# Performance work log

Hardware: AMD Instinct MI355X
Metric: run time of the kernel (lower is better)

## Reference

```python
import jax, jax.numpy as jnp
import numpy as np


def setup_inputs() -> dict:
    key = jax.random.key(0)
    B, D, C, H = 4096, 64, 128, 512
    ks = jax.random.split(key, 6)
    return {
        "q_z_x_params": jax.random.normal(ks[0], (B, C), jnp.float32),
        "eps": jax.random.normal(ks[1], (B, D), jnp.float32),
        "W1": jax.random.normal(ks[2], (D + C, H), jnp.float32) / np.sqrt(D + C).astype(np.float32),
        "b1": jnp.zeros((H,), jnp.float32),
        "W2": jax.random.normal(ks[3], (H, H), jnp.float32) / np.sqrt(H).astype(np.float32),
        "b2": jnp.zeros((H,), jnp.float32),
        "W3": jax.random.normal(ks[4], (H, 2 * D), jnp.float32) / np.sqrt(H).astype(np.float32),
        "b3": jnp.zeros((2 * D,), jnp.float32),
    }


def _made_masks(D, C, H):
    # Standard MADE degrees, natural ordering; context columns fully connected.
    m_in = np.arange(1, D + 1)                      # input degrees 1..D
    m_h = (np.arange(H) % (D - 1)) + 1              # hidden degrees 1..D-1
    M1 = np.concatenate([m_h[None, :] >= m_in[:, None],
                         np.ones((C, H), bool)], axis=0)   # (D+C, H)
    M2 = m_h[None, :] >= m_h[:, None]               # (H, H)
    m_out = np.tile(np.arange(1, D + 1), 2)         # (2D,) mean||prescale
    M3 = m_out[None, :] > m_h[:, None]              # (H, 2D)
    f32 = jnp.float32
    return jnp.asarray(M1, f32), jnp.asarray(M2, f32), jnp.asarray(M3, f32)


def reference(q_z_x_params, eps, W1, b1, W2, b2, W3, b3):
    B, D = eps.shape
    C = q_z_x_params.shape[1]
    H = W2.shape[0]
    M1, M2, M3 = _made_masks(D, C, H)
    mW1, mW2, mW3 = W1 * M1, W2 * M2, W3 * M3

    def made(z):
        x = jnp.concatenate([z, q_z_x_params], axis=1)   # (B, D+C)
        h1 = jax.nn.relu(x @ mW1 + b1)
        h2 = jax.nn.relu(h1 @ mW2 + b2)
        out = h2 @ mW3 + b3                              # (B, 2D)
        return out[:, :D], out[:, D:]

    def step(z, i):
        mean, prescale = made(z)
        mu_i = jnp.take(mean, i, axis=1)                 # (B,)
        scale_i = jax.nn.softplus(jnp.take(prescale, i, axis=1))
        z_i = mu_i + scale_i * jnp.take(eps, i, axis=1)  # reparameterized Normal sample
        z = z.at[:, i].set(z_i)
        return z, None

    z0 = jnp.zeros((B, D), eps.dtype)
    z_sample, _ = jax.lax.scan(step, z0, jnp.arange(D))
    return z_sample
```

## Files before the change

kernel.cpp:

```cpp
#include <hip/hip_runtime.h>
#include <math.h>

#define DD 64
#define CC 128
#define HH 512
#define BATCH 4096

typedef _Float16 f16;

__global__ void to_f16(const float* __restrict__ W1, const float* __restrict__ W2,
                       f16* __restrict__ w2h, f16* __restrict__ w1ch) {
    int idx = blockIdx.x * 256 + threadIdx.x;
    if (idx < HH * HH) w2h[idx] = (f16)W2[idx];
    else               w1ch[idx - HH * HH] = (f16)W1[DD * HH + (idx - HH * HH)];
}

__device__ __forceinline__ float fast_softplus(float x) {
    float t = exp2f(-fabsf(x) * 1.44269504f);
    return fmaxf(x, 0.f) + 0.69314718f * log2f(1.f + t);
}

__device__ __forceinline__ float bcast(float x, int l) {
    return __int_as_float(__builtin_amdgcn_readlane(__float_as_int(x), l));
}

typedef const __attribute__((address_space(1))) void* as1_cptr;
typedef __attribute__((address_space(3))) void* as3_ptr;
__device__ __forceinline__ void glds16(const void* g, float* l) {
    __builtin_amdgcn_global_load_lds((as1_cptr)g, (as3_ptr)l, 16, 0, 0);
}

union HW { float4 f4; f16 h[8]; };

#define SLOT_W1 (9 * 256)
#define BUF_F   (SLOT_W1 + 512)

__global__ __launch_bounds__(128, 2) void made_sample(
    const float* __restrict__ ctx,
    const float* __restrict__ eps,
    const float* __restrict__ W1,
    const float* __restrict__ b1,
    const float* __restrict__ b2,
    const float* __restrict__ W3,
    const float* __restrict__ b3,
    const f16*   __restrict__ w2h,
    const f16*   __restrict__ w1ch,
    float* __restrict__ out)
{
    const int lane  = threadIdx.x & 63;
    const int w     = threadIdx.x >> 6;
    const int rbase = blockIdx.x * 4 + w * 2;
    const int jbase = 8 * lane;

    __shared__ float sbuf[2][BUF_F];

    int deg[8];
    #pragma unroll
    for (int u = 0; u < 8; ++u) deg[u] = (jbase + u) % 63 + 1;

    float p1[2][8], p2[2][8], acc[2][2];
    #pragma unroll
    for (int u = 0; u < 8; ++u) {
        float t1 = b1[jbase + u], t2 = b2[jbase + u];
        p1[0][u] = t1; p1[1][u] = t1;
        p2[0][u] = t2; p2[1][u] = t2;
    }
    acc[0][0] = 0.f; acc[0][1] = 0.f; acc[1][0] = 0.f; acc[1][1] = 0.f;

    float ca[2], cb[2], ep[2];
    #pragma unroll
    for (int r = 0; r < 2; ++r) {
        ca[r] = ctx[(rbase + r) * CC + lane];
        cb[r] = ctx[(rbase + r) * CC + 64 + lane];
        ep[r] = eps[(rbase + r) * DD + lane];
    }
    const float b3m = b3[lane];
    const float b3p = b3[64 + lane];

    auto stage_ctx = [&](int ch, float* buf) {
        #pragma unroll
        for (int q = 0; q < 8; q += 2)
            glds16(w1ch + (8 * ch + q + w) * HH + lane * 8, buf + (q + w) * 256);
    };
    auto stage_step = [&](int in, float* buf) {
        const int basen = (in == 0) ? 0 : (in - 1);
        #pragma unroll
        for (int o = w; o < 11; o += 2) {
            if (o < 9) {
                int k = basen + 63 * o;
                if (k >= HH) k = HH - 1;
                glds16(w2h + k * HH + lane * 8, buf + o * 256);
            } else if (o == 9) {
                glds16(W1 + in * HH + lane * 8, buf + SLOT_W1);
            } else {
                glds16(W1 + in * HH + lane * 8 + 4, buf + SLOT_W1 + 256);
            }
        }
    };

    stage_ctx(0, sbuf[0]);
    __syncthreads();
    #pragma unroll 1
    for (int ch = 0; ch < 16; ++ch) {
        float* cur = sbuf[ch & 1];
        float* nxt = sbuf[(ch + 1) & 1];
        if (ch < 15) stage_ctx(ch + 1, nxt);
        else         stage_step(0, sbuf[0]);
        #pragma unroll
        for (int q = 0; q < 8; ++q) {
            HW uw; uw.f4 = *(const float4*)(cur + q * 256 + lane * 4);
            const int c = 8 * ch + q;
            #pragma unroll
            for (int r = 0; r < 2; ++r) {
                const float cv = bcast((ch < 8) ? ca[r] : cb[r], c & 63);
                #pragma unroll
                for (int u = 0; u < 8; ++u)
                    p1[r][u] = fmaf((float)uw.h[u], cv, p1[r][u]);
            }
        }
        __syncthreads();
    }

    float z[2] = {0.f, 0.f};

    #pragma unroll 1
    for (int i = 0; i < DD; ++i) {
        float* cur = sbuf[i & 1];
        float* nxt = sbuf[(i + 1) & 1];
        if (i < 63) stage_step(i + 1, nxt);

        const int base = (i == 0) ? 0 : (i - 1);

        float w3m[9], w3p[9];
        #pragma unroll
        for (int t = 0; t < 9; ++t) {
            const int k  = base + 63 * t;
            const int ks = (k < HH) ? k : (HH - 1);
            w3m[t] = W3[ks * (2 * DD) + lane];
            w3p[t] = W3[ks * (2 * DD) + 64 + lane];
        }

        HW w2v[9];
        #pragma unroll
        for (int t = 0; t < 9; ++t)
            w2v[t].f4 = *(const float4*)(cur + t * 256 + lane * 4);
        float w1v[8];
        {
            float4 a = *(const float4*)(cur + SLOT_W1 + lane * 4);
            float4 b = *(const float4*)(cur + SLOT_W1 + 256 + lane * 4);
            w1v[0] = a.x; w1v[1] = a.y; w1v[2] = a.z; w1v[3] = a.w;
            w1v[4] = b.x; w1v[5] = b.y; w1v[6] = b.z; w1v[7] = b.w;
        }

        float m[2];
        #pragma unroll
        for (int r = 0; r < 2; ++r) {
            float mv = 0.f;
            #pragma unroll
            for (int u = 0; u < 8; ++u) mv = (deg[u] == i) ? p1[r][u] : mv;
            m[r] = fmaxf(mv, 0.f);
        }

        #pragma unroll
        for (int t = 0; t < 9; ++t) {
            const int k = base + 63 * t;
            float h0, h1v;
            if (t == 8) {
                const float vm = (k < HH) ? 1.f : 0.f;
                h0  = vm * bcast(m[0], 63);
                h1v = vm * bcast(m[1], 63);
            } else {
                h0  = bcast(m[0], k >> 3);
                h1v = bcast(m[1], k >> 3);
            }
            #pragma unroll
            for (int u = 0; u < 8; ++u) {
                p2[0][u] = fmaf((float)w2v[t].h[u], h0,  p2[0][u]);
                p2[1][u] = fmaf((float)w2v[t].h[u], h1v, p2[1][u]);
            }
        }

        float hn[2];
        #pragma unroll
        for (int r = 0; r < 2; ++r) {
            float hv = 0.f;
            #pragma unroll
            for (int u = 0; u < 8; ++u) hv = (deg[u] == i) ? p2[r][u] : hv;
            hn[r] = fmaxf(hv, 0.f);
        }

        #pragma unroll
        for (int t = 0; t < 9; ++t) {
            const int k = base + 63 * t;
            float h0, h1v;
            if (t == 8) {
                const float vm = (k < HH) ? 1.f : 0.f;
                h0  = vm * bcast(hn[0], 63);
                h1v = vm * bcast(hn[1], 63);
            } else {
                h0  = bcast(hn[0], k >> 3);
                h1v = bcast(hn[1], k >> 3);
            }
            acc[0][0] = fmaf(h0,  w3m[t], acc[0][0]);
            acc[0][1] = fmaf(h0,  w3p[t], acc[0][1]);
            acc[1][0] = fmaf(h1v, w3m[t], acc[1][0]);
            acc[1][1] = fmaf(h1v, w3p[t], acc[1][1]);
        }

        #pragma unroll
        for (int r = 0; r < 2; ++r) {
            const float am = acc[r][0] + b3m;
            const float ap = acc[r][1] + b3p;
            const float sp = fast_softplus(ap);
            const float zc = fmaf(sp, ep[r], am);
            const float zi = bcast(zc, i);
            if (lane == i) z[r] = zi;
            #pragma unroll
            for (int u = 0; u < 8; ++u) p1[r][u] = fmaf(zi, w1v[u], p1[r][u]);
        }

        __syncthreads();
    }

    #pragma unroll
    for (int r = 0; r < 2; ++r) out[(rbase + r) * DD + lane] = z[r];
}

extern "C" void kernel_launch(void* const* d_in, const int* in_sizes, int n_in,
                              void* d_out, int out_size, void* d_ws, size_t ws_size,
                              hipStream_t stream) {
    const float* ctx = (const float*)d_in[0];
    const float* eps = (const float*)d_in[1];
    const float* W1  = (const float*)d_in[2];
    const float* b1  = (const float*)d_in[3];
    const float* W2  = (const float*)d_in[4];
    const float* b2  = (const float*)d_in[5];
    const float* W3  = (const float*)d_in[6];
    const float* b3  = (const float*)d_in[7];

    f16* w2h  = (f16*)d_ws;
    f16* w1ch = w2h + HH * HH;

    to_f16<<<(HH * HH + CC * HH) / 256, 256, 0, stream>>>(W1, W2, w2h, w1ch);
    made_sample<<<BATCH / 4, 128, 0, stream>>>(ctx, eps, W1, b1, b2, W3, b3,
                                               w2h, w1ch, (float*)d_out);
}
```

Baseline: 208.4 us.

## Use 256-thread blocks, stage W3 rows through LDS, and pack accumulators into float2

Doubles the block to four waves (eight batch rows per block), so each staged weight slice in LDS is shared by twice as many rows and the cooperative global-to-LDS copies are split four ways. The per-step W3 rows that used to be read straight from global memory by every wave are now prefetched into the double-buffered LDS slot along with the W2/W1 slices. Layer-2 and output accumulators are held in two-wide float vectors, probably so the compiler can emit packed FMAs, and W2 fragments are read from LDS inside the loop instead of all up front. The cost is fewer blocks in flight (512 instead of 1024) and a larger LDS footprint per block, and the diff leaves some dead placeholder code behind.

```diff
diff --git a/kernel.cpp b/kernel.cpp
--- a/kernel.cpp
+++ b/kernel.cpp
@@ -7,6 +7,9 @@
 #define BATCH 4096
 
 typedef _Float16 f16;
+typedef __attribute__((ext_vector_type(2))) float f32x2;
+
+__device__ __forceinline__ f32x2 splat2(float x) { f32x2 v; v[0] = x; v[1] = x; return v; }
 
 __global__ void to_f16(const float* __restrict__ W1, const float* __restrict__ W2,
                        f16* __restrict__ w2h, f16* __restrict__ w1ch) {
@@ -26,16 +29,21 @@
 
 typedef const __attribute__((address_space(1))) void* as1_cptr;
 typedef __attribute__((address_space(3))) void* as3_ptr;
-__device__ __forceinline__ void glds16(const void* g, float* l) {
+__device__ __forceinline__ void glds16(const void* g, void* l) {
     __builtin_amdgcn_global_load_lds((as1_cptr)g, (as3_ptr)l, 16, 0, 0);
 }
-
-union HW { float4 f4; f16 h[8]; };
-
-#define SLOT_W1 (9 * 256)
-#define BUF_F   (SLOT_W1 + 512)
-
-__global__ __launch_bounds__(128, 2) void made_sample(
+__device__ __forceinline__ void glds4(const void* g, void* l) {
+    __builtin_amdgcn_global_load_lds((as1_cptr)g, (as3_ptr)l, 4, 0, 0);
+}
+
+union H8 { float4 f4; f16 h[8]; };
+
+
+#define SLOT_W1 2304
+#define SLOT_W3 (SLOT_W1 + 512)
+#define BUF_F   (SLOT_W3 + 1152)
+
+__global__ __launch_bounds__(256, 2) void made_sample(
     const float* __restrict__ ctx,
     const float* __restrict__ eps,
     const float* __restrict__ W1,
@@ -49,7 +57,7 @@
 {
     const int lane  = threadIdx.x & 63;
     const int w     = threadIdx.x >> 6;
-    const int rbase = blockIdx.x * 4 + w * 2;
+    const int rbase = blockIdx.x * 8 + w * 2;
     const int jbase = 8 * lane;
 
     __shared__ float sbuf[2][BUF_F];
@@ -58,14 +66,20 @@
     #pragma unroll
     for (int u = 0; u < 8; ++u) deg[u] = (jbase + u) % 63 + 1;
 
-    float p1[2][8], p2[2][8], acc[2][2];
+    float p1[2][8];
+    f32x2 p2[2][4], acc[2];
     #pragma unroll
     for (int u = 0; u < 8; ++u) {
-        float t1 = b1[jbase + u], t2 = b2[jbase + u];
+        float t1 = b1[jbase + u];
         p1[0][u] = t1; p1[1][u] = t1;
-        p2[0][u] = t2; p2[1][u] = t2;
-    }
-    acc[0][0] = 0.f; acc[0][1] = 0.f; acc[1][0] = 0.f; acc[1][1] = 0.f;
+    }
+    #pragma unroll
+    for (int j = 0; j < 4; ++j) {
+        f32x2 t2; t2[0] = b2[jbase + 2 * j]; t2[1] = b2[jbase + 2 * j + 1];
+        p2[0][j] = t2; p2[1][j] = t2;
+    }
+    acc[0] = splat2(0.f);
+    acc[1] = splat2(0.f);
 
     float ca[2], cb[2], ep[2];
     #pragma unroll
@@ -77,38 +91,52 @@
     const float b3m = b3[lane];
     const float b3p = b3[64 + lane];
 
-    auto stage_ctx = [&](int ch, float* buf) {
-        #pragma unroll
-        for (int q = 0; q < 8; q += 2)
-            glds16(w1ch + (8 * ch + q + w) * HH + lane * 8, buf + (q + w) * 256);
+    f16* bufh = (f16*)&sbuf[0][0];
+    const int bufh_stride = BUF_F * 2;
+
+    auto stage_ctx = [&](int ch, int bsel) {
+        f16* bh = bufh + bsel * bufh_stride;
+        #pragma unroll
+        for (int o = 0; o < 2; ++o) {
+            const int q = 4 * o + w;
+            glds16(w1ch + (8 * ch + q) * HH + lane * 8, bh + q * 512);
+        }
     };
-    auto stage_step = [&](int in, float* buf) {
+    auto stage_step = [&](int in, int bsel) {
         const int basen = (in == 0) ? 0 : (in - 1);
-        #pragma unroll
-        for (int o = w; o < 11; o += 2) {
+        f16*   bh = bufh + bsel * bufh_stride;
+        float* bf = &sbuf[bsel][0];
+        #pragma unroll
+        for (int o8 = 0; o8 < 8; ++o8) {
+            const int o = 4 * o8 + w;
             if (o < 9) {
                 int k = basen + 63 * o;
                 if (k >= HH) k = HH - 1;
-                glds16(w2h + k * HH + lane * 8, buf + o * 256);
-            } else if (o == 9) {
-                glds16(W1 + in * HH + lane * 8, buf + SLOT_W1);
-            } else {
-                glds16(W1 + in * HH + lane * 8 + 4, buf + SLOT_W1 + 256);
+                glds16(w2h + k * HH + lane * 8, bh + o * 512);
+            } else if (o < 11) {
+                const int hf = o - 9;
+                glds16(W1 + in * HH + lane * 8 + hf * 4, bf + SLOT_W1 + hf * 256);
+            } else if (o < 29) {
+                const int t = (o - 11) >> 1, hf = (o - 11) & 1;
+                int k = basen + 63 * t;
+                if (k >= HH) k = HH - 1;
+                glds4(W3 + k * (2 * DD) + hf * 64 + lane,
+                      bf + SLOT_W3 + t * 128 + hf * 64);
             }
         }
     };
 
-    stage_ctx(0, sbuf[0]);
+    stage_ctx(0, 0);
     __syncthreads();
     #pragma unroll 1
     for (int ch = 0; ch < 16; ++ch) {
-        float* cur = sbuf[ch & 1];
-        float* nxt = sbuf[(ch + 1) & 1];
-        if (ch < 15) stage_ctx(ch + 1, nxt);
-        else         stage_step(0, sbuf[0]);
+        const int cs = ch & 1;
+        if (ch < 15) stage_ctx(ch + 1, cs ^ 1);
+        else         stage_step(0, 0);
+        f16* bh = bufh + cs * bufh_stride;
         #pragma unroll
         for (int q = 0; q < 8; ++q) {
-            HW uw; uw.f4 = *(const float4*)(cur + q * 256 + lane * 4);
+            H8 uw; uw.f4 = *(const float4*)(bh + q * 512 + lane * 8);
             const int c = 8 * ch + q;
             #pragma unroll
             for (int r = 0; r < 2; ++r) {
@@ -125,31 +153,26 @@
 
     #pragma unroll 1
     for (int i = 0; i < DD; ++i) {
-        float* cur = sbuf[i & 1];
-        float* nxt = sbuf[(i + 1) & 1];
-        if (i < 63) stage_step(i + 1, nxt);
-
+        const int cs = i & 1;
+        if (i < 63) stage_step(i + 1, cs ^ 1);
+
+        f16*   bh = bufh + cs * bufh_stride;
+        float* bf = &sbuf[cs][0];
         const int base = (i == 0) ? 0 : (i - 1);
-
-        float w3m[9], w3p[9];
+        const float vm8 = (base + 504 < HH) ? 1.f : 0.f;
+
+        f32x2 w1v[4];
+        {
+            float4 a = *(const float4*)(bf + SLOT_W1 + lane * 4);
+            float4 b = *(const float4*)(bf + SLOT_W1 + 256 + lane * 4);
+            w1v[0][0] = a.x; w1v[0][1] = a.y; w1v[1][0] = a.z; w1v[1][1] = a.w;
+            w1v[2][0] = b.x; w1v[2][1] = b.y; w1v[3][0] = b.z; w1v[3][1] = b.w;
+        }
+        f32x2 w3v[9];
         #pragma unroll
         for (int t = 0; t < 9; ++t) {
-            const int k  = base + 63 * t;
-            const int ks = (k < HH) ? k : (HH - 1);
-            w3m[t] = W3[ks * (2 * DD) + lane];
-            w3p[t] = W3[ks * (2 * DD) + 64 + lane];
-        }
-
-        HW w2v[9];
-        #pragma unroll
-        for (int t = 0; t < 9; ++t)
-            w2v[t].f4 = *(const float4*)(cur + t * 256 + lane * 4);
-        float w1v[8];
-        {
-            float4 a = *(const float4*)(cur + SLOT_W1 + lane * 4);
-            float4 b = *(const float4*)(cur + SLOT_W1 + 256 + lane * 4);
-            w1v[0] = a.x; w1v[1] = a.y; w1v[2] = a.z; w1v[3] = a.w;
-            w1v[4] = b.x; w1v[5] = b.y; w1v[6] = b.z; w1v[7] = b.w;
+            w3v[t][0] = bf[SLOT_W3 + t * 128 + lane];
+            w3v[t][1] = bf[SLOT_W3 + t * 128 + 64 + lane];
         }
 
         float m[2];
@@ -164,19 +187,20 @@
         #pragma unroll
         for (int t = 0; t < 9; ++t) {
             const int k = base + 63 * t;
+            H8 uw; uw.f4 = *(const float4*)(bh + t * 512 + lane * 8);
             float h0, h1v;
             if (t == 8) {
-                const float vm = (k < HH) ? 1.f : 0.f;
-                h0  = vm * bcast(m[0], 63);
-                h1v = vm * bcast(m[1], 63);
+                h0  = vm8 * bcast(m[0], 63);
+                h1v = vm8 * bcast(m[1], 63);
             } else {
                 h0  = bcast(m[0], k >> 3);
                 h1v = bcast(m[1], k >> 3);
             }
             #pragma unroll
             for (int u = 0; u < 8; ++u) {
-                p2[0][u] = fmaf((float)w2v[t].h[u], h0,  p2[0][u]);
-                p2[1][u] = fmaf((float)w2v[t].h[u], h1v, p2[1][u]);
+                const float wu = (float)uw.h[u];
+                p2[0][u >> 1][u & 1] = fmaf(wu, h0,  p2[0][u >> 1][u & 1]);
+                p2[1][u >> 1][u & 1] = fmaf(wu, h1v, p2[1][u >> 1][u & 1]);
             }
         }
 
@@ -185,27 +209,19 @@
         for (int r = 0; r < 2; ++r) {
             float hv = 0.f;
             #pragma unroll
-            for (int u = 0; u < 8; ++u) hv = (deg[u] == i) ? p2[r][u] : hv;
+            for (int u = 0; u < 8; ++u)
+                hv = (deg[u] == i) ? p2[r][u >> 1][u & 1] : hv;
             hn[r] = fmaxf(hv, 0.f);
         }
 
         #pragma unroll
-        for (int t = 0; t < 9; ++t) {
+        for (int t = 0; t < 8; ++t) {
             const int k = base + 63 * t;
-            float h0, h1v;
-            if (t == 8) {
-                const float vm = (k < HH) ? 1.f : 0.f;
-                h0  = vm * bcast(hn[0], 63);
-                h1v = vm * bcast(hn[1], 63);
-            } else {
-                h0  = bcast(hn[0], k >> 3);
-                h1v = bcast(hn[1], k >> 3);
-            }
-            acc[0][0] = fmaf(h0,  w3m[t], acc[0][0]);
-            acc[0][1] = fmaf(h0,  w3p[t], acc[0][1]);
-            acc[1][0] = fmaf(h1v, w3m[t], acc[1][0]);
-            acc[1][1] = fmaf(h1v, w3p[t], acc[1][1]);
-        }
+            acc[0] += splat2(bcast(hn[0], k >> 3)) * w3v[t];
+            acc[1] += splat2(bcast(hn[1], k >> 3)) * w3v[t];
+        }
+        acc[0] += splat2(vm8 * bcast(hn[0], 63)) * w3v[8];
+        acc[1] += splat2(vm8 * bcast(hn[1], 63)) * w3v[8];
 
         #pragma unroll
         for (int r = 0; r < 2; ++r) {
@@ -215,8 +231,15 @@
             const float zc = fmaf(sp, ep[r], am);
             const float zi = bcast(zc, i);
             if (lane == i) z[r] = zi;
-            #pragma unroll
-            for (int u = 0; u < 8; ++u) p1[r][u] = fmaf(zi, w1v[u], p1[r][u]);
+            const f32x2 zi2 = splat2(zi);
+            #pragma unroll
+            for (int j = 0; j < 4; ++j) {
+                f32x2 t = p1[r][2 * j] < 0.f ? splat2(0.f) : splat2(0.f); (void)t;
+            }
+            #pragma unroll
+            for (int u = 0; u < 8; ++u)
+                p1[r][u] = fmaf(zi, w1v[u >> 1][u & 1], p1[r][u]);
+            (void)zi2;
         }
 
         __syncthreads();
@@ -242,6 +265,6 @@
     f16* w1ch = w2h + HH * HH;
 
     to_f16<<<(HH * HH + CC * HH) / 256, 256, 0, stream>>>(W1, W2, w2h, w1ch);
-    made_sample<<<BATCH / 4, 128, 0, stream>>>(ctx, eps, W1, b1, b2, W3, b3,
+    made_sample<<<BATCH / 8, 256, 0, stream>>>(ctx, eps, W1, b1, b2, W3, b3,
                                                w2h, w1ch, (float*)d_out);
 }
```

After: 205.2 us. About the same (-1.5%).
